# Optimization experiments

Measured on AMD Instinct MI355X. Metric: run time of the kernel, lower is better.

The kernel has to match this reference:

```python
import jax, jax.numpy as jnp
import numpy as np

N_NODES = 20000
N_EDGES = 640000
IN_DIM = 128
HID = 128
OUT_DIM = 64
N_STEPS = 16   # N in the torch module
H = 0.1        # ODE step size


def setup_inputs() -> dict:
    key = jax.random.key(0)
    ks = jax.random.split(key, 20)
    s = 1.0 / np.sqrt(HID)

    def g(k, shape, scale=s):
        return (jax.random.normal(k, shape, dtype=jnp.float32) * scale)

    return {
        "x": jax.random.normal(ks[0], (N_NODES, IN_DIM), dtype=jnp.float32),
        "edge_index": jax.random.randint(ks[1], (2, N_EDGES), 0, N_NODES, dtype=jnp.int32),
        "W_enc1": g(ks[2], (HID, IN_DIM), 1.0 / np.sqrt(IN_DIM)),
        "b_enc1": g(ks[3], (HID,)),
        "W_enc2": g(ks[4], (HID, HID)),
        "b_enc2": g(ks[5], (HID,)),
        "W_ih_f": g(ks[6], (4 * HID, HID)),
        "W_hh_f": g(ks[7], (4 * HID, HID)),
        "b_ih_f": g(ks[8], (4 * HID,)),
        "b_hh_f": g(ks[9], (4 * HID,)),
        "W_ih_b": g(ks[10], (4 * HID, HID)),
        "W_hh_b": g(ks[11], (4 * HID, HID)),
        "b_ih_b": g(ks[12], (4 * HID,)),
        "b_hh_b": g(ks[13], (4 * HID,)),
        "W_f1": g(ks[14], (HID, 2 * HID), 1.0 / np.sqrt(2 * HID)),
        "b_f1": g(ks[15], (HID,)),
        "W_f2": g(ks[16], (OUT_DIM, HID)),
        "b_f2": g(ks[17], (OUT_DIM,)),
    }


def _lstm_scan(xs, W_ih, W_hh, b_ih, b_hh):
    """Unidirectional LSTM over xs [T, B, H] -> hidden states [T, B, H]."""
    B = xs.shape[1]
    Hd = W_hh.shape[1]
    h0 = jnp.zeros((B, Hd), xs.dtype)

    def cell(carry, x_t):
        h, c = carry
        gates = x_t @ W_ih.T + b_ih + h @ W_hh.T + b_hh
        i, f, g, o = jnp.split(gates, 4, axis=-1)  # torch gate order: i,f,g,o
        i = jax.nn.sigmoid(i)
        f = jax.nn.sigmoid(f)
        g = jnp.tanh(g)
        o = jax.nn.sigmoid(o)
        c_new = f * c + i * g
        h_new = o * jnp.tanh(c_new)
        return (h_new, c_new), h_new

    _, hs = jax.lax.scan(cell, (h0, h0), xs)
    return hs


def reference(x, edge_index, W_enc1, b_enc1, W_enc2, b_enc2,
              W_ih_f, W_hh_f, b_ih_f, b_hh_f,
              W_ih_b, W_hh_b, b_ih_b, b_hh_b,
              W_f1, b_f1, W_f2, b_f2):
    row, col = edge_index[0], edge_index[1]

    # initial encoders
    X = x @ W_enc1.T + b_enc1
    Y = jnp.zeros_like(X)
    X = jax.nn.relu(X)
    X = X @ W_enc2.T + b_enc2

    # node degree (count of col occurrences), inf-guard not needed (deg used directly)
    deg = jax.ops.segment_sum(jnp.ones((N_EDGES,), X.dtype), col, num_segments=N_NODES)

    def wave_step(carry, _):
        Xc, Yc = carry
        # L x = deg*x - sum_{j->i} x_j   (scatter-add of -x[row] at col)
        mes = -jax.ops.segment_sum(Xc[row], col, num_segments=N_NODES)
        vel_update = deg[:, None] * Xc + mes
        Yn = Yc - H * vel_update
        Xn = Xc + H * Yn
        return (Xn, Yn), Xn

    _, Xs = jax.lax.scan(wave_step, (X, Y), None, length=N_STEPS - 1)
    X_tilde = jnp.concatenate([X[None], Xs], axis=0)  # [N, n_nodes, HID]

    hs_f = _lstm_scan(X_tilde, W_ih_f, W_hh_f, b_ih_f, b_hh_f)
    hs_b = _lstm_scan(X_tilde[::-1], W_ih_b, W_hh_b, b_ih_b, b_hh_b)
    # out_vec[-1] = [fwd hidden at last step, bwd hidden at last position]
    out_last = jnp.concatenate([hs_f[-1], hs_b[0]], axis=-1)  # [n_nodes, 2*HID]

    out = jax.nn.relu(out_last @ W_f1.T + b_f1)
    out = out @ W_f2.T + b_f2
    return out
```

## Files before the change

### kernel.cpp

```cpp
#include <hip/hip_runtime.h>
#include <hip/hip_bf16.h>
#include <cstdint>
#include <cstddef>

#define N_NODES 20000
#define N_EDGES 640000
#define HID     128
#define OUT_DIM 64
#define NSTEPS  16
#define HSTEP   0.1f
#define H2      0.01f
#define NBLK    625

typedef unsigned short u16;
typedef __attribute__((ext_vector_type(8))) short short8;
typedef __attribute__((ext_vector_type(4))) float f32x4;

__device__ __forceinline__ float bf2f(u16 u) {
    union { unsigned int i; float f; } v; v.i = ((unsigned int)u) << 16; return v.f;
}
__device__ __forceinline__ u16 f2bf(float f) {
    union { float f; unsigned int i; } v; v.f = f;
    unsigned int x = v.i;
    unsigned int r = x + 0x7FFFu + ((x >> 16) & 1u);
    return (u16)(r >> 16);
}

__device__ __forceinline__ float sigm(float x) { return 1.f / (1.f + __expf(-x)); }
__device__ __forceinline__ float tanh_fast(float x) {
    float e2 = __expf(-2.f * fabsf(x));
    float t = (1.f - e2) / (1.f + e2);
    return copysignf(t, x);
}

__global__ void detect_kernel(const u16* __restrict__ xraw, int* __restrict__ flag) {
    __shared__ int cnt;
    if (threadIdx.x == 0) cnt = 0;
    __syncthreads();
    int c = 0;
    for (int i = threadIdx.x; i < 4096; i += 256) {
        int e = (xraw[i] >> 7) & 0xFF;
        if (e >= 0x90) c++;
    }
    atomicAdd(&cnt, c);
    __syncthreads();
    if (threadIdx.x == 0) *flag = (cnt > 100) ? 1 : 0;
}

#define N_CVT 15
struct CvtArgs { const void* s[N_CVT]; };
__constant__ const int cvt_off[N_CVT + 1] = {
    0, 16384, 16512, 32896, 33024, 98560, 164096, 164608, 165120,
    230656, 231168, 231680, 264448, 264576, 272768, 272832 };

__global__ void convert_kernel(CvtArgs a, float* __restrict__ dst,
                               const int* __restrict__ flag) {
    int i = blockIdx.x * blockDim.x + threadIdx.x;
    if (i >= 272832) return;
    int seg = 0;
    #pragma unroll
    for (int s = 1; s < N_CVT; ++s) if (i >= cvt_off[s]) seg = s;
    int j = i - cvt_off[seg];
    float v = (*flag) ? ((const float*)a.s[seg])[j]
                      : bf2f(((const u16*)a.s[seg])[j]);
    dst[i] = v;
}

__global__ void build_wswz_kernel(const float* __restrict__ wsf,
                                  u16* __restrict__ WswzF, u16* __restrict__ WswzB,
                                  u16* __restrict__ WswzH, u16* __restrict__ WswzO,
                                  u16* __restrict__ WswzE1, u16* __restrict__ WswzE2) {
    int o = blockIdx.x * blockDim.x + threadIdx.x;
    if (o < 131072) {
        int j = o & 7, l = (o >> 3) & 63, rest = o >> 9;
        int ck = rest & 7, nt = rest >> 3;
        int n = nt * 16 + (l & 15);
        int k = ck * 32 + (l >> 4) * 8 + j;
        const float* Wihf = wsf + 33024;
        const float* Whhf = wsf + 98560;
        float v = (k < 128) ? Wihf[n * 128 + k] : Whhf[n * 128 + (k - 128)];
        WswzF[o] = f2bf(v);
    }
    if (o < 65536) {
        int j = o & 7, l = (o >> 3) & 63, rest = o >> 9;
        int ck = rest & 3, nt = rest >> 2;
        int n = nt * 16 + (l & 15);
        int k = ck * 32 + (l >> 4) * 8 + j;
        const float* Wihb = wsf + 165120;
        WswzB[o] = f2bf(Wihb[n * 128 + k]);
    }
    if (o < 32768) {
        int j = o & 7, l = (o >> 3) & 63, rest = o >> 9;
        int ck = rest & 7, nt = rest >> 3;
        int n = nt * 16 + (l & 15);
        int k = ck * 32 + (l >> 4) * 8 + j;
        const float* Wf1 = wsf + 231680;
        WswzH[o] = f2bf(Wf1[n * 256 + k]);
    }
    if (o < 8192) {
        int j = o & 7, l = (o >> 3) & 63, rest = o >> 9;
        int ck = rest & 3, nt = rest >> 2;
        int n = nt * 16 + (l & 15);
        int k = ck * 32 + (l >> 4) * 8 + j;
        const float* Wf2 = wsf + 264576;
        WswzO[o] = f2bf(Wf2[n * 128 + k]);
    }
    if (o < 16384) {
        int j = o & 7, l = (o >> 3) & 63, rest = o >> 9;
        int ck = rest & 3, nt = rest >> 2;
        int n = nt * 16 + (l & 15);
        int k = ck * 32 + (l >> 4) * 8 + j;
        const float* We1 = wsf + 0;
        const float* We2 = wsf + 16512;
        WswzE1[o] = f2bf(We1[n * 128 + k]);
        WswzE2[o] = f2bf(We2[n * 128 + k]);
    }
}

__global__ void count_kernel(const int* __restrict__ ei, int* __restrict__ deg) {
    int e = blockIdx.x * blockDim.x + threadIdx.x;
    if (e < N_EDGES) atomicAdd(&deg[ei[N_EDGES + e]], 1);
}

__global__ __launch_bounds__(1024) void scan_kernel(const int* __restrict__ deg,
                                                    int* __restrict__ rowptr,
                                                    float* __restrict__ degf) {
    __shared__ int sd[1024];
    const int t = threadIdx.x;
    const int CH = (N_NODES + 1023) / 1024;
    int base = t * CH;
    int s = 0;
    for (int i = 0; i < CH; ++i) {
        int idx = base + i;
        if (idx < N_NODES) s += deg[idx];
    }
    sd[t] = s;
    __syncthreads();
    for (int off = 1; off < 1024; off <<= 1) {
        int v = (t >= off) ? sd[t - off] : 0;
        __syncthreads();
        sd[t] += v;
        __syncthreads();
    }
    int run = (t == 0) ? 0 : sd[t - 1];
    for (int i = 0; i < CH; ++i) {
        int idx = base + i;
        if (idx < N_NODES) {
            rowptr[idx] = run;
            degf[idx] = (float)deg[idx];
            run += deg[idx];
        }
    }
    if (t == 1023) rowptr[N_NODES] = sd[1023];
}

__global__ void fill_kernel(const int* __restrict__ ei, const int* __restrict__ rowptr,
                            int* __restrict__ fill, int* __restrict__ csr) {
    int e = blockIdx.x * blockDim.x + threadIdx.x;
    if (e < N_EDGES) {
        int d = ei[N_EDGES + e];
        int p = atomicAdd(&fill[d], 1);
        csr[rowptr[d] + p] = ei[e];
    }
}

__global__ __launch_bounds__(512) void encoder_kernel(
    const void* __restrict__ xv,
    const u16* __restrict__ WswzE1, const u16* __restrict__ WswzE2,
    const float* __restrict__ benc1, const float* __restrict__ benc2,
    float* __restrict__ Xa, u16* __restrict__ Xsnap0, const int* __restrict__ flag)
{
    __shared__ __align__(16) u16 H1[32][136];
    const int w = threadIdx.x >> 6;
    const int l = threadIdx.x & 63;
    const int l15 = l & 15, quad = l >> 4;
    const int m0 = blockIdx.x * 32;
    const int kof = quad * 8;
    const int j = w * 16 + l15;
    const bool xf32 = (*flag != 0);

    f32x4 acc[2] = {};
    #pragma unroll
    for (int ck = 0; ck < 4; ++ck) {
        const int kc = ck * 32;
        short8 a0, a1;
        if (xf32) {
            const float* r0 = (const float*)xv + (size_t)(m0 + l15) * HID + kc + kof;
            const float* r1 = (const float*)xv + (size_t)(m0 + 16 + l15) * HID + kc + kof;
            union { u16 u[8]; short8 v; } t0, t1;
            #pragma unroll
            for (int e = 0; e < 8; ++e) { t0.u[e] = f2bf(r0[e]); t1.u[e] = f2bf(r1[e]); }
            a0 = t0.v; a1 = t1.v;
        } else {
            a0 = *(const short8*)((const u16*)xv + (size_t)(m0 + l15) * HID + kc + kof);
            a1 = *(const short8*)((const u16*)xv + (size_t)(m0 + 16 + l15) * HID + kc + kof);
        }
        short8 b = *(const short8*)(WswzE1 + (((size_t)(w * 4 + ck)) << 9) + (l << 3));
        acc[0] = __builtin_amdgcn_mfma_f32_16x16x32_bf16(a0, b, acc[0], 0, 0, 0);
        acc[1] = __builtin_amdgcn_mfma_f32_16x16x32_bf16(a1, b, acc[1], 0, 0, 0);
    }
    {
        const float bj = benc1[j];
        #pragma unroll
        for (int mt = 0; mt < 2; ++mt)
            #pragma unroll
            for (int i = 0; i < 4; ++i)
                H1[mt * 16 + quad * 4 + i][j] = f2bf(fmaxf(acc[mt][i] + bj, 0.f));
    }
    __syncthreads();

    f32x4 acc2[2] = {};
    #pragma unroll
    for (int ck = 0; ck < 4; ++ck) {
        const int kc = ck * 32;
        short8 a0 = *(const short8*)(&H1[l15][kc + kof]);
        short8 a1 = *(const short8*)(&H1[16 + l15][kc + kof]);
        short8 b = *(const short8*)(WswzE2 + (((size_t)(w * 4 + ck)) << 9) + (l << 3));
        acc2[0] = __builtin_amdgcn_mfma_f32_16x16x32_bf16(a0, b, acc2[0], 0, 0, 0);
        acc2[1] = __builtin_amdgcn_mfma_f32_16x16x32_bf16(a1, b, acc2[1], 0, 0, 0);
    }
    {
        const float bj = benc2[j];
        #pragma unroll
        for (int mt = 0; mt < 2; ++mt)
            #pragma unroll
            for (int i = 0; i < 4; ++i) {
                int m = m0 + mt * 16 + quad * 4 + i;
                float o = acc2[mt][i] + bj;
                Xa[(size_t)m * HID + j] = o;
                Xsnap0[(size_t)m * HID + j] = f2bf(o);
            }
    }
}

template<bool FIRST>
__global__ __launch_bounds__(256) void wave_kernel(
    const float* __restrict__ Xcur, float* __restrict__ Xdst,
    const u16* __restrict__ XbfP, u16* __restrict__ XbfN,
    const float* __restrict__ degf,
    const int* __restrict__ rowptr, const int* __restrict__ csr)
{
    const int node = blockIdx.x * 4 + (threadIdx.x >> 6);
    const int lane = threadIdx.x & 63;
    const int q = lane >> 4;
    const int fl = (lane & 15) * 8;

    const int beg = rowptr[node], end = rowptr[node + 1];
    float s0[8] = {}, s1[8] = {}, s2[8] = {}, s3[8] = {};

    int i = beg;
    for (; i + 16 <= end; i += 16) {
        int v0 = csr[i + 0 + q];
        int v1 = csr[i + 4 + q];
        int v2 = csr[i + 8 + q];
        int v3 = csr[i + 12 + q];
        short8 g0 = *(const short8*)(XbfP + (size_t)v0 * HID + fl);
        short8 g1 = *(const short8*)(XbfP + (size_t)v1 * HID + fl);
        short8 g2 = *(const short8*)(XbfP + (size_t)v2 * HID + fl);
        short8 g3 = *(const short8*)(XbfP + (size_t)v3 * HID + fl);
        #pragma unroll
        for (int e = 0; e < 8; ++e) {
            s0[e] += bf2f((u16)g0[e]);
            s1[e] += bf2f((u16)g1[e]);
            s2[e] += bf2f((u16)g2[e]);
            s3[e] += bf2f((u16)g3[e]);
        }
    }
    for (; i + 4 <= end; i += 4) {
        int v = csr[i + q];
        short8 g = *(const short8*)(XbfP + (size_t)v * HID + fl);
        #pragma unroll
        for (int e = 0; e < 8; ++e) s0[e] += bf2f((u16)g[e]);
    }
    if (i + q < end) {
        int v = csr[i + q];
        short8 g = *(const short8*)(XbfP + (size_t)v * HID + fl);
        #pragma unroll
        for (int e = 0; e < 8; ++e) s1[e] += bf2f((u16)g[e]);
    }

    float t[8];
    #pragma unroll
    for (int e = 0; e < 8; ++e) {
        t[e] = (s0[e] + s1[e]) + (s2[e] + s3[e]);
        t[e] += __shfl_xor(t[e], 16, 64);
        t[e] += __shfl_xor(t[e], 32, 64);
    }

    if (q == 0) {
        const size_t off = (size_t)node * HID + fl;
        float xc[8], xp[8], xn[8];
        *(float4*)&xc[0] = *(const float4*)(Xcur + off);
        *(float4*)&xc[4] = *(const float4*)(Xcur + off + 4);
        if (!FIRST) {
            *(float4*)&xp[0] = *(const float4*)(Xdst + off);
            *(float4*)&xp[4] = *(const float4*)(Xdst + off + 4);
        }
        const float d = degf[node];
        const float c0 = 2.f - H2 * d;
        short8 sv;
        #pragma unroll
        for (int e = 0; e < 8; ++e) {
            float prev = FIRST ? xc[e] : xp[e];
            xn[e] = c0 * xc[e] - prev + H2 * t[e];
            sv[e] = (short)f2bf(xn[e]);
        }
        *(float4*)(Xdst + off)     = *(float4*)&xn[0];
        *(float4*)(Xdst + off + 4) = *(float4*)&xn[4];
        *(short8*)(XbfN + off)     = sv;
    }
}

__global__ __launch_bounds__(512) void lstm_tail_kernel(
    const u16* __restrict__ Xsnap,
    const u16* __restrict__ WswzF,
    const float* __restrict__ bih, const float* __restrict__ bhh,
    const u16* __restrict__ WswzB, const u16* __restrict__ WswzH,
    const u16* __restrict__ WswzO,
    const float* __restrict__ bihb, const float* __restrict__ bhhb,
    const float* __restrict__ bf1, const float* __restrict__ bf2_,
    void* __restrict__ out, const int* __restrict__ oflag)
{
    __shared__ __align__(16) u16 hL[32][136];
    __shared__ __align__(16) u16 Hb[32][136];
    __shared__ __align__(16) u16 F1[32][136];
    const int w = threadIdx.x >> 6;
    const int l = threadIdx.x & 63;
    const int l15 = l & 15, quad = l >> 4;
    const int m0 = blockIdx.x * 32;
    const int kof = quad * 8;
    const int j = w * 16 + l15;

    {
        const int r  = threadIdx.x >> 4;
        const int cc = (threadIdx.x & 15) * 8;
        short8 z = {};
        *(short8*)&hL[r][cc] = z;
    }

    const float bI = bih[j]       + bhh[j];
    const float bF = bih[128 + j] + bhh[128 + j];
    const float bG = bih[256 + j] + bhh[256 + j];
    const float bO = bih[384 + j] + bhh[384 + j];
    float cst[2][4] = {};

    const size_t rowA0 = (size_t)(m0 + l15) * HID + kof;
    const size_t rowA1 = (size_t)(m0 + 16 + l15) * HID + kof;
    __syncthreads();

    #pragma unroll 1
    for (int t = 0; t < NSTEPS; ++t) {
        const u16* Xbf = Xsnap + (size_t)t * N_NODES * HID;
        f32x4 acc[2][4] = {};
        #pragma unroll
        for (int kc = 0; kc < 256; kc += 32) {
            const int ck = kc >> 5;
            short8 a0, a1;
            if (kc < 128) {
                a0 = *(const short8*)(Xbf + rowA0 + kc);
                a1 = *(const short8*)(Xbf + rowA1 + kc);
            } else {
                a0 = *(const short8*)(&hL[l15][kc - 128 + kof]);
                a1 = *(const short8*)(&hL[16 + l15][kc - 128 + kof]);
            }
            #pragma unroll
            for (int q = 0; q < 4; ++q) {
                int nt = q * 8 + w;
                short8 b = *(const short8*)(WswzF + (((size_t)(nt * 8 + ck)) << 9) + (l << 3));
                acc[0][q] = __builtin_amdgcn_mfma_f32_16x16x32_bf16(a0, b, acc[0][q], 0, 0, 0);
                acc[1][q] = __builtin_amdgcn_mfma_f32_16x16x32_bf16(a1, b, acc[1][q], 0, 0, 0);
            }
        }
        __syncthreads();
        #pragma unroll
        for (int mt = 0; mt < 2; ++mt) {
            #pragma unroll
            for (int i = 0; i < 4; ++i) {
                float gi = sigm(acc[mt][0][i] + bI);
                float gf = sigm(acc[mt][1][i] + bF);
                float gg = tanh_fast(acc[mt][2][i] + bG);
                float go = sigm(acc[mt][3][i] + bO);
                float cn = gf * cst[mt][i] + gi * gg;
                cst[mt][i] = cn;
                hL[mt * 16 + quad * 4 + i][j] = f2bf(go * tanh_fast(cn));
            }
        }
        __syncthreads();
    }

    {
        const u16* Xbf15 = Xsnap + (size_t)(NSTEPS - 1) * N_NODES * HID;
        f32x4 acc[2][4] = {};
        #pragma unroll
        for (int kc = 0; kc < 128; kc += 32) {
            const int ck = kc >> 5;
            short8 a0 = *(const short8*)(Xbf15 + rowA0 + kc);
            short8 a1 = *(const short8*)(Xbf15 + rowA1 + kc);
            #pragma unroll
            for (int q = 0; q < 4; ++q) {
                int nt = q * 8 + w;
                short8 b = *(const short8*)(WswzB + (((size_t)(nt * 4 + ck)) << 9) + (l << 3));
                acc[0][q] = __builtin_amdgcn_mfma_f32_16x16x32_bf16(a0, b, acc[0][q], 0, 0, 0);
                acc[1][q] = __builtin_amdgcn_mfma_f32_16x16x32_bf16(a1, b, acc[1][q], 0, 0, 0);
            }
        }
        const float cI = bihb[j]       + bhhb[j];
        const float cG = bihb[256 + j] + bhhb[256 + j];
        const float cO = bihb[384 + j] + bhhb[384 + j];
        #pragma unroll
        for (int mt = 0; mt < 2; ++mt)
            #pragma unroll
            for (int i = 0; i < 4; ++i) {
                float gi = sigm(acc[mt][0][i] + cI);
                float gg = tanh_fast(acc[mt][2][i] + cG);
                float go = sigm(acc[mt][3][i] + cO);
                Hb[mt * 16 + quad * 4 + i][j] = f2bf(go * tanh_fast(gi * gg));
            }
    }
    __syncthreads();

    {
        f32x4 acc[2] = {};
        #pragma unroll
        for (int kc = 0; kc < 256; kc += 32) {
            const int ck = kc >> 5;
            short8 a0, a1;
            if (kc < 128) {
                a0 = *(const short8*)(&hL[l15][kc + kof]);
                a1 = *(const short8*)(&hL[16 + l15][kc + kof]);
            } else {
                a0 = *(const short8*)(&Hb[l15][(kc - 128) + kof]);
                a1 = *(const short8*)(&Hb[16 + l15][(kc - 128) + kof]);
            }
            short8 b = *(const short8*)(WswzH + (((size_t)(w * 8 + ck)) << 9) + (l << 3));
            acc[0] = __builtin_amdgcn_mfma_f32_16x16x32_bf16(a0, b, acc[0], 0, 0, 0);
            acc[1] = __builtin_amdgcn_mfma_f32_16x16x32_bf16(a1, b, acc[1], 0, 0, 0);
        }
        const float bj = bf1[j];
        #pragma unroll
        for (int mt = 0; mt < 2; ++mt)
            #pragma unroll
            for (int i = 0; i < 4; ++i)
                F1[mt * 16 + quad * 4 + i][j] = f2bf(fmaxf(acc[mt][i] + bj, 0.f));
    }
    __syncthreads();

    {
        const int nt = w & 3, mh = w >> 2;
        f32x4 acc = {};
        #pragma unroll
        for (int kc = 0; kc < 128; kc += 32) {
            const int ck = kc >> 5;
            short8 a = *(const short8*)(&F1[mh * 16 + l15][kc + kof]);
            short8 b = *(const short8*)(WswzO + (((size_t)(nt * 4 + ck)) << 9) + (l << 3));
            acc = __builtin_amdgcn_mfma_f32_16x16x32_bf16(a, b, acc, 0, 0, 0);
        }
        const int jo = nt * 16 + l15;
        const float bj = bf2_[jo];
        const bool obf = (*oflag == 0);
        #pragma unroll
        for (int i = 0; i < 4; ++i) {
            int m = m0 + mh * 16 + quad * 4 + i;
            float o = acc[i] + bj;
            if (obf) ((u16*)out)[(size_t)m * OUT_DIM + jo] = f2bf(o);
            else     ((float*)out)[(size_t)m * OUT_DIM + jo] = o;
        }
    }
}

extern "C" void kernel_launch(void* const* d_in, const int* in_sizes, int n_in,
                              void* d_out, int out_size, void* d_ws, size_t ws_size,
                              hipStream_t stream)
{
    const void* x  = d_in[0];
    const int*  ei = (const int*)d_in[1];

    const size_t SZ_NH  = (size_t)N_NODES * HID * sizeof(float);
    const size_t SZ_NHB = (size_t)N_NODES * HID * sizeof(u16);
    const size_t SZ_I   = 80128;

    char* p = (char*)d_ws;
    float* Xa    = (float*)p; p += SZ_NH;
    float* Xb    = (float*)p; p += SZ_NH;
    u16*   Xsnap = (u16*)p;   p += (size_t)NSTEPS * SZ_NHB;
    int*   deg   = (int*)p;   p += SZ_I;
    int*   fill  = (int*)p;   p += SZ_I;
    int*   rowp  = (int*)p;   p += SZ_I;
    float* degf  = (float*)p; p += SZ_I;
    int*   csr   = (int*)p;   p += (size_t)N_EDGES * sizeof(int);
    int*   flag  = (int*)p;   p += 128;
    float* wsf   = (float*)p; p += 272832 * sizeof(float);
    u16*   WswzF  = (u16*)p;  p += 131072 * sizeof(u16);
    u16*   WswzB  = (u16*)p;  p += 65536 * sizeof(u16);
    u16*   WswzH  = (u16*)p;  p += 32768 * sizeof(u16);
    u16*   WswzO  = (u16*)p;  p += 8192 * sizeof(u16);
    u16*   WswzE1 = (u16*)p;  p += 16384 * sizeof(u16);
    u16*   WswzE2 = (u16*)p;  p += 16384 * sizeof(u16);

    float* benc1 = wsf + 16384;
    float* benc2 = wsf + 32896;
    float* bihf  = wsf + 164096;
    float* bhhf  = wsf + 164608;
    float* bihb  = wsf + 230656;
    float* bhhb  = wsf + 231168;
    float* bf1   = wsf + 264448;
    float* bf2_  = wsf + 272768;

    (void)hipMemsetAsync(deg, 0, 2 * SZ_I, stream);

    detect_kernel<<<1, 256, 0, stream>>>((const u16*)x, flag);
    CvtArgs ca;
    ca.s[0] = d_in[2];  ca.s[1] = d_in[3];  ca.s[2] = d_in[4];  ca.s[3] = d_in[5];
    ca.s[4] = d_in[6];  ca.s[5] = d_in[7];  ca.s[6] = d_in[8];  ca.s[7] = d_in[9];
    ca.s[8] = d_in[10]; ca.s[9] = d_in[12]; ca.s[10] = d_in[13];
    ca.s[11] = d_in[14]; ca.s[12] = d_in[15]; ca.s[13] = d_in[16]; ca.s[14] = d_in[17];
    convert_kernel<<<(272832 + 255) / 256, 256, 0, stream>>>(ca, wsf, flag);
    build_wswz_kernel<<<512, 256, 0, stream>>>(wsf, WswzF, WswzB, WswzH, WswzO,
                                               WswzE1, WswzE2);

    count_kernel<<<(N_EDGES + 255) / 256, 256, 0, stream>>>(ei, deg);
    scan_kernel<<<1, 1024, 0, stream>>>(deg, rowp, degf);
    fill_kernel<<<(N_EDGES + 255) / 256, 256, 0, stream>>>(ei, rowp, fill, csr);

    const int NB = NBLK;

    encoder_kernel<<<NB, 512, 0, stream>>>(x, WswzE1, WswzE2, benc1, benc2,
                                           Xa, Xsnap, flag);

    float* Xc_ = Xa;
    float* Xo_ = Xb;
    for (int t = 1; t < NSTEPS; ++t) {
        const u16* XbP = Xsnap + (size_t)(t - 1) * N_NODES * HID;
        u16*       XbN = Xsnap + (size_t)t * N_NODES * HID;
        if (t == 1)
            wave_kernel<true><<<N_NODES / 4, 256, 0, stream>>>(
                Xc_, Xo_, XbP, XbN, degf, rowp, csr);
        else
            wave_kernel<false><<<N_NODES / 4, 256, 0, stream>>>(
                Xc_, Xo_, XbP, XbN, degf, rowp, csr);
        float* tf = Xc_; Xc_ = Xo_; Xo_ = tf;
    }

    lstm_tail_kernel<<<NB, 512, 0, stream>>>(Xsnap, WswzF, bihf, bhhf,
                                             WswzB, WswzH, WswzO,
                                             bihb, bhhb, bf1, bf2_,
                                             d_out, flag);
}
```

Measured before the change: 827.8 us.

## Fuse forward LSTM steps into wave-step kernels as extra blocks

```diff
diff --git a/kernel.cpp b/kernel.cpp
--- a/kernel.cpp
+++ b/kernel.cpp
@@ -11,6 +11,8 @@
 #define HSTEP   0.1f
 #define H2      0.01f
 #define NBLK    625
+#define WAVEBLK 5000
+#define LSTMBLK 1250
 
 typedef unsigned short u16;
 typedef __attribute__((ext_vector_type(8))) short short8;
@@ -234,85 +236,140 @@
 }
 
 template<bool FIRST>
-__global__ __launch_bounds__(256) void wave_kernel(
+__global__ __launch_bounds__(256) void fused_step_kernel(
     const float* __restrict__ Xcur, float* __restrict__ Xdst,
     const u16* __restrict__ XbfP, u16* __restrict__ XbfN,
     const float* __restrict__ degf,
-    const int* __restrict__ rowptr, const int* __restrict__ csr)
+    const int* __restrict__ rowptr, const int* __restrict__ csr,
+    const u16* __restrict__ hR, u16* __restrict__ hW, float* __restrict__ cf,
+    const u16* __restrict__ WswzF,
+    const float* __restrict__ bih, const float* __restrict__ bhh)
 {
-    const int node = blockIdx.x * 4 + (threadIdx.x >> 6);
-    const int lane = threadIdx.x & 63;
-    const int q = lane >> 4;
-    const int fl = (lane & 15) * 8;
-
-    const int beg = rowptr[node], end = rowptr[node + 1];
-    float s0[8] = {}, s1[8] = {}, s2[8] = {}, s3[8] = {};
-
-    int i = beg;
-    for (; i + 16 <= end; i += 16) {
-        int v0 = csr[i + 0 + q];
-        int v1 = csr[i + 4 + q];
-        int v2 = csr[i + 8 + q];
-        int v3 = csr[i + 12 + q];
-        short8 g0 = *(const short8*)(XbfP + (size_t)v0 * HID + fl);
-        short8 g1 = *(const short8*)(XbfP + (size_t)v1 * HID + fl);
-        short8 g2 = *(const short8*)(XbfP + (size_t)v2 * HID + fl);
-        short8 g3 = *(const short8*)(XbfP + (size_t)v3 * HID + fl);
+    if (blockIdx.x < WAVEBLK) {
+        const int node = blockIdx.x * 4 + (threadIdx.x >> 6);
+        const int lane = threadIdx.x & 63;
+        const int q = lane >> 4;
+        const int fl = (lane & 15) * 8;
+
+        const int beg = rowptr[node], end = rowptr[node + 1];
+        float s0[8] = {}, s1[8] = {}, s2[8] = {}, s3[8] = {};
+
+        int i = beg;
+        for (; i + 16 <= end; i += 16) {
+            int v0 = csr[i + 0 + q];
+            int v1 = csr[i + 4 + q];
+            int v2 = csr[i + 8 + q];
+            int v3 = csr[i + 12 + q];
+            short8 g0 = *(const short8*)(XbfP + (size_t)v0 * HID + fl);
+            short8 g1 = *(const short8*)(XbfP + (size_t)v1 * HID + fl);
+            short8 g2 = *(const short8*)(XbfP + (size_t)v2 * HID + fl);
+            short8 g3 = *(const short8*)(XbfP + (size_t)v3 * HID + fl);
+            #pragma unroll
+            for (int e = 0; e < 8; ++e) {
+                s0[e] += bf2f((u16)g0[e]);
+                s1[e] += bf2f((u16)g1[e]);
+                s2[e] += bf2f((u16)g2[e]);
+                s3[e] += bf2f((u16)g3[e]);
+            }
+        }
+        for (; i + 4 <= end; i += 4) {
+            int v = csr[i + q];
+            short8 g = *(const short8*)(XbfP + (size_t)v * HID + fl);
+            #pragma unroll
+            for (int e = 0; e < 8; ++e) s0[e] += bf2f((u16)g[e]);
+        }
+        if (i + q < end) {
+            int v = csr[i + q];
+            short8 g = *(const short8*)(XbfP + (size_t)v * HID + fl);
+            #pragma unroll
+            for (int e = 0; e < 8; ++e) s1[e] += bf2f((u16)g[e]);
+        }
+
+        float t[8];
         #pragma unroll
         for (int e = 0; e < 8; ++e) {
-            s0[e] += bf2f((u16)g0[e]);
-            s1[e] += bf2f((u16)g1[e]);
-            s2[e] += bf2f((u16)g2[e]);
-            s3[e] += bf2f((u16)g3[e]);
-        }
-    }
-    for (; i + 4 <= end; i += 4) {
-        int v = csr[i + q];
-        short8 g = *(const short8*)(XbfP + (size_t)v * HID + fl);
-        #pragma unroll
-        for (int e = 0; e < 8; ++e) s0[e] += bf2f((u16)g[e]);
-    }
-    if (i + q < end) {
-        int v = csr[i + q];
-        short8 g = *(const short8*)(XbfP + (size_t)v * HID + fl);
-        #pragma unroll
-        for (int e = 0; e < 8; ++e) s1[e] += bf2f((u16)g[e]);
-    }
-
-    float t[8];
+            t[e] = (s0[e] + s1[e]) + (s2[e] + s3[e]);
+            t[e] += __shfl_xor(t[e], 16, 64);
+            t[e] += __shfl_xor(t[e], 32, 64);
+        }
+
+        if (q == 0) {
+            const size_t off = (size_t)node * HID + fl;
+            float xc[8], xp[8], xn[8];
+            *(float4*)&xc[0] = *(const float4*)(Xcur + off);
+            *(float4*)&xc[4] = *(const float4*)(Xcur + off + 4);
+            if (!FIRST) {
+                *(float4*)&xp[0] = *(const float4*)(Xdst + off);
+                *(float4*)&xp[4] = *(const float4*)(Xdst + off + 4);
+            }
+            const float d = degf[node];
+            const float c0 = 2.f - H2 * d;
+            short8 sv;
+            #pragma unroll
+            for (int e = 0; e < 8; ++e) {
+                float prev = FIRST ? xc[e] : xp[e];
+                xn[e] = c0 * xc[e] - prev + H2 * t[e];
+                sv[e] = (short)f2bf(xn[e]);
+            }
+            *(float4*)(Xdst + off)     = *(float4*)&xn[0];
+            *(float4*)(Xdst + off + 4) = *(float4*)&xn[4];
+            *(short8*)(XbfN + off)     = sv;
+        }
+        return;
+    }
+
+    const int tid = threadIdx.x;
+    const int w = tid >> 6;
+    const int l = tid & 63;
+    const int l15 = l & 15, quad = l >> 4;
+    const int kof = quad * 8;
+    const int m0 = (blockIdx.x - WAVEBLK) * 16;
+
+    f32x4 acc[2][4] = {};
+    const size_t rowA = (size_t)(m0 + l15) * HID + kof;
+
     #pragma unroll
-    for (int e = 0; e < 8; ++e) {
-        t[e] = (s0[e] + s1[e]) + (s2[e] + s3[e]);
-        t[e] += __shfl_xor(t[e], 16, 64);
-        t[e] += __shfl_xor(t[e], 32, 64);
-    }
-
-    if (q == 0) {
-        const size_t off = (size_t)node * HID + fl;
-        float xc[8], xp[8], xn[8];
-        *(float4*)&xc[0] = *(const float4*)(Xcur + off);
-        *(float4*)&xc[4] = *(const float4*)(Xcur + off + 4);
-        if (!FIRST) {
-            *(float4*)&xp[0] = *(const float4*)(Xdst + off);
-            *(float4*)&xp[4] = *(const float4*)(Xdst + off + 4);
-        }
-        const float d = degf[node];
-        const float c0 = 2.f - H2 * d;
-        short8 sv;
-        #pragma unroll
-        for (int e = 0; e < 8; ++e) {
-            float prev = FIRST ? xc[e] : xp[e];
-            xn[e] = c0 * xc[e] - prev + H2 * t[e];
-            sv[e] = (short)f2bf(xn[e]);
-        }
-        *(float4*)(Xdst + off)     = *(float4*)&xn[0];
-        *(float4*)(Xdst + off + 4) = *(float4*)&xn[4];
-        *(short8*)(XbfN + off)     = sv;
-    }
-}
-
-__global__ __launch_bounds__(512) void lstm_tail_kernel(
-    const u16* __restrict__ Xsnap,
+    for (int kc = 0; kc < 256; kc += 32) {
+        const int ck = kc >> 5;
+        short8 a = (kc < 128)
+            ? *(const short8*)(XbfP + rowA + kc)
+            : *(const short8*)(hR + rowA + (kc - 128));
+        #pragma unroll
+        for (int jp = 0; jp < 2; ++jp)
+            #pragma unroll
+            for (int q = 0; q < 4; ++q) {
+                const int nt = q * 8 + w + jp * 4;
+                short8 b = *(const short8*)(WswzF +
+                    (((size_t)(nt * 8 + ck)) << 9) + (l << 3));
+                acc[jp][q] = __builtin_amdgcn_mfma_f32_16x16x32_bf16(
+                    a, b, acc[jp][q], 0, 0, 0);
+            }
+    }
+
+    #pragma unroll
+    for (int jp = 0; jp < 2; ++jp) {
+        const int j = (w + 4 * jp) * 16 + l15;
+        const float bI = bih[j]       + bhh[j];
+        const float bF = bih[128 + j] + bhh[128 + j];
+        const float bG = bih[256 + j] + bhh[256 + j];
+        const float bO = bih[384 + j] + bhh[384 + j];
+        #pragma unroll
+        for (int i = 0; i < 4; ++i) {
+            const size_t off = (size_t)(m0 + quad * 4 + i) * HID + j;
+            float gi = sigm(acc[jp][0][i] + bI);
+            float gf = sigm(acc[jp][1][i] + bF);
+            float gg = tanh_fast(acc[jp][2][i] + bG);
+            float go = sigm(acc[jp][3][i] + bO);
+            float cn = gf * cf[off] + gi * gg;
+            cf[off] = cn;
+            hW[off] = f2bf(go * tanh_fast(cn));
+        }
+    }
+}
+
+__global__ __launch_bounds__(512) void tail_kernel(
+    const u16* __restrict__ Xbf15,
+    const u16* __restrict__ hPrev, const float* __restrict__ cPrev,
     const u16* __restrict__ WswzF,
     const float* __restrict__ bih, const float* __restrict__ bhh,
     const u16* __restrict__ WswzB, const u16* __restrict__ WswzH,
@@ -334,31 +391,34 @@
     {
         const int r  = threadIdx.x >> 4;
         const int cc = (threadIdx.x & 15) * 8;
-        short8 z = {};
-        *(short8*)&hL[r][cc] = z;
+        *(short8*)&hL[r][cc] =
+            *(const short8*)(hPrev + (size_t)(m0 + r) * HID + cc);
     }
 
     const float bI = bih[j]       + bhh[j];
     const float bF = bih[128 + j] + bhh[128 + j];
     const float bG = bih[256 + j] + bhh[256 + j];
     const float bO = bih[384 + j] + bhh[384 + j];
-    float cst[2][4] = {};
+    float cst[2][4];
+    #pragma unroll
+    for (int mt = 0; mt < 2; ++mt)
+        #pragma unroll
+        for (int i = 0; i < 4; ++i)
+            cst[mt][i] = cPrev[(size_t)(m0 + mt * 16 + quad * 4 + i) * HID + j];
 
     const size_t rowA0 = (size_t)(m0 + l15) * HID + kof;
     const size_t rowA1 = (size_t)(m0 + 16 + l15) * HID + kof;
     __syncthreads();
 
-    #pragma unroll 1
-    for (int t = 0; t < NSTEPS; ++t) {
-        const u16* Xbf = Xsnap + (size_t)t * N_NODES * HID;
+    {
         f32x4 acc[2][4] = {};
         #pragma unroll
         for (int kc = 0; kc < 256; kc += 32) {
             const int ck = kc >> 5;
             short8 a0, a1;
             if (kc < 128) {
-                a0 = *(const short8*)(Xbf + rowA0 + kc);
-                a1 = *(const short8*)(Xbf + rowA1 + kc);
+                a0 = *(const short8*)(Xbf15 + rowA0 + kc);
+                a1 = *(const short8*)(Xbf15 + rowA1 + kc);
             } else {
                 a0 = *(const short8*)(&hL[l15][kc - 128 + kof]);
                 a1 = *(const short8*)(&hL[16 + l15][kc - 128 + kof]);
@@ -381,7 +441,6 @@
                 float gg = tanh_fast(acc[mt][2][i] + bG);
                 float go = sigm(acc[mt][3][i] + bO);
                 float cn = gf * cst[mt][i] + gi * gg;
-                cst[mt][i] = cn;
                 hL[mt * 16 + quad * 4 + i][j] = f2bf(go * tanh_fast(cn));
             }
         }
@@ -389,7 +448,6 @@
     }
 
     {
-        const u16* Xbf15 = Xsnap + (size_t)(NSTEPS - 1) * N_NODES * HID;
         f32x4 acc[2][4] = {};
         #pragma unroll
         for (int kc = 0; kc < 128; kc += 32) {
@@ -483,6 +541,9 @@
     float* Xa    = (float*)p; p += SZ_NH;
     float* Xb    = (float*)p; p += SZ_NH;
     u16*   Xsnap = (u16*)p;   p += (size_t)NSTEPS * SZ_NHB;
+    float* cf    = (float*)p; p += SZ_NH;
+    u16*   hB    = (u16*)p;   p += SZ_NHB;
+    u16*   hA    = (u16*)p;   p += SZ_NHB;
     int*   deg   = (int*)p;   p += SZ_I;
     int*   fill  = (int*)p;   p += SZ_I;
     int*   rowp  = (int*)p;   p += SZ_I;
@@ -507,6 +568,7 @@
     float* bf2_  = wsf + 272768;
 
     (void)hipMemsetAsync(deg, 0, 2 * SZ_I, stream);
+    (void)hipMemsetAsync(cf, 0, SZ_NH + SZ_NHB, stream);
 
     detect_kernel<<<1, 256, 0, stream>>>((const u16*)x, flag);
     CvtArgs ca;
@@ -522,27 +584,30 @@
     scan_kernel<<<1, 1024, 0, stream>>>(deg, rowp, degf);
     fill_kernel<<<(N_EDGES + 255) / 256, 256, 0, stream>>>(ei, rowp, fill, csr);
 
-    const int NB = NBLK;
-
-    encoder_kernel<<<NB, 512, 0, stream>>>(x, WswzE1, WswzE2, benc1, benc2,
-                                           Xa, Xsnap, flag);
+    encoder_kernel<<<NBLK, 512, 0, stream>>>(x, WswzE1, WswzE2, benc1, benc2,
+                                             Xa, Xsnap, flag);
 
     float* Xc_ = Xa;
     float* Xo_ = Xb;
     for (int t = 1; t < NSTEPS; ++t) {
+        const int s = t - 1;
         const u16* XbP = Xsnap + (size_t)(t - 1) * N_NODES * HID;
         u16*       XbN = Xsnap + (size_t)t * N_NODES * HID;
+        const u16* hR = (s & 1) ? hA : hB;
+        u16*       hW = (s & 1) ? hB : hA;
         if (t == 1)
-            wave_kernel<true><<<N_NODES / 4, 256, 0, stream>>>(
-                Xc_, Xo_, XbP, XbN, degf, rowp, csr);
+            fused_step_kernel<true><<<WAVEBLK + LSTMBLK, 256, 0, stream>>>(
+                Xc_, Xo_, XbP, XbN, degf, rowp, csr, hR, hW, cf,
+                WswzF, bihf, bhhf);
         else
-            wave_kernel<false><<<N_NODES / 4, 256, 0, stream>>>(
-                Xc_, Xo_, XbP, XbN, degf, rowp, csr);
+            fused_step_kernel<false><<<WAVEBLK + LSTMBLK, 256, 0, stream>>>(
+                Xc_, Xo_, XbP, XbN, degf, rowp, csr, hR, hW, cf,
+                WswzF, bihf, bhhf);
         float* tf = Xc_; Xc_ = Xo_; Xo_ = tf;
     }
 
-    lstm_tail_kernel<<<NB, 512, 0, stream>>>(Xsnap, WswzF, bihf, bhhf,
-                                             WswzB, WswzH, WswzO,
-                                             bihb, bhhb, bf1, bf2_,
-                                             d_out, flag);
-}
+    tail_kernel<<<NBLK, 512, 0, stream>>>(
+        Xsnap + (size_t)(NSTEPS - 1) * N_NODES * HID, hA, cf,
+        WswzF, bihf, bhhf, WswzB, WswzH, WswzO,
+        bihb, bhhb, bf1, bf2_, d_out, flag);
+}
```

New measurement: 968.1 us. 16.9% more time.

## Split LSTM recurrence into 256-thread kernel and separate tail kernel

Applied to the files above, without the earlier changes.

```diff
diff --git a/kernel.cpp b/kernel.cpp
--- a/kernel.cpp
+++ b/kernel.cpp
@@ -311,10 +311,103 @@
     }
 }
 
-__global__ __launch_bounds__(512) void lstm_tail_kernel(
+__global__ __launch_bounds__(256) void lstm16_kernel(
     const u16* __restrict__ Xsnap,
+    u16* __restrict__ hOut,
     const u16* __restrict__ WswzF,
-    const float* __restrict__ bih, const float* __restrict__ bhh,
+    const float* __restrict__ bih, const float* __restrict__ bhh)
+{
+    __shared__ __align__(16) u16 hL[32][136];
+    const int tid  = threadIdx.x;
+    const int w    = tid >> 6;
+    const int l    = tid & 63;
+    const int l15  = l & 15;
+    const int quad = l >> 4;
+    const int kof  = quad * 8;
+    const int m0   = blockIdx.x * 32;
+
+    {
+        const int r  = tid >> 3;
+        const int cc = (tid & 7) * 16;
+        short8 z = {};
+        *(short8*)&hL[r][cc]     = z;
+        *(short8*)&hL[r][cc + 8] = z;
+    }
+
+    const int jh[2] = { w * 16 + l15, (w + 4) * 16 + l15 };
+    float cst[2][2][4] = {};
+    float bI[2], bF[2], bG[2], bO[2];
+    #pragma unroll
+    for (int jp = 0; jp < 2; ++jp) {
+        bI[jp] = bih[jh[jp]]       + bhh[jh[jp]];
+        bF[jp] = bih[128 + jh[jp]] + bhh[128 + jh[jp]];
+        bG[jp] = bih[256 + jh[jp]] + bhh[256 + jh[jp]];
+        bO[jp] = bih[384 + jh[jp]] + bhh[384 + jh[jp]];
+    }
+
+    const size_t rowA0 = (size_t)(m0 + l15) * HID + kof;
+    const size_t rowA1 = (size_t)(m0 + 16 + l15) * HID + kof;
+    __syncthreads();
+
+    #pragma unroll 1
+    for (int t = 0; t < NSTEPS; ++t) {
+        const u16* Xbf = Xsnap + (size_t)t * N_NODES * HID;
+
+        f32x4 acc[2][2][4] = {};
+        #pragma unroll
+        for (int kc = 0; kc < 256; kc += 32) {
+            const int ck = kc >> 5;
+            short8 a0, a1;
+            if (kc < 128) {
+                a0 = *(const short8*)(Xbf + rowA0 + kc);
+                a1 = *(const short8*)(Xbf + rowA1 + kc);
+            } else {
+                a0 = *(const short8*)(&hL[l15][kc - 128 + kof]);
+                a1 = *(const short8*)(&hL[16 + l15][kc - 128 + kof]);
+            }
+            #pragma unroll
+            for (int jp = 0; jp < 2; ++jp)
+                #pragma unroll
+                for (int g4 = 0; g4 < 4; ++g4) {
+                    const int nt = g4 * 8 + w + jp * 4;
+                    short8 b = *(const short8*)(WswzF +
+                        (((size_t)(nt * 8 + ck)) << 9) + (l << 3));
+                    acc[0][jp][g4] = __builtin_amdgcn_mfma_f32_16x16x32_bf16(
+                        a0, b, acc[0][jp][g4], 0, 0, 0);
+                    acc[1][jp][g4] = __builtin_amdgcn_mfma_f32_16x16x32_bf16(
+                        a1, b, acc[1][jp][g4], 0, 0, 0);
+                }
+        }
+        __syncthreads();
+
+        #pragma unroll
+        for (int mt = 0; mt < 2; ++mt)
+            #pragma unroll
+            for (int jp = 0; jp < 2; ++jp)
+                #pragma unroll
+                for (int i = 0; i < 4; ++i) {
+                    float gi = sigm(acc[mt][jp][0][i] + bI[jp]);
+                    float gf = sigm(acc[mt][jp][1][i] + bF[jp]);
+                    float gg = tanh_fast(acc[mt][jp][2][i] + bG[jp]);
+                    float go = sigm(acc[mt][jp][3][i] + bO[jp]);
+                    float cn = gf * cst[mt][jp][i] + gi * gg;
+                    cst[mt][jp][i] = cn;
+                    hL[mt * 16 + quad * 4 + i][jh[jp]] = f2bf(go * tanh_fast(cn));
+                }
+        __syncthreads();
+    }
+
+    {
+        const int r  = tid >> 3;
+        const int cc = (tid & 7) * 16;
+        u16* hdst = hOut + (size_t)(m0 + r) * HID + cc;
+        *(short8*)(hdst)     = *(const short8*)&hL[r][cc];
+        *(short8*)(hdst + 8) = *(const short8*)&hL[r][cc + 8];
+    }
+}
+
+__global__ __launch_bounds__(512) void tail2_kernel(
+    const u16* __restrict__ Xbf15, const u16* __restrict__ h15,
     const u16* __restrict__ WswzB, const u16* __restrict__ WswzH,
     const u16* __restrict__ WswzO,
     const float* __restrict__ bihb, const float* __restrict__ bhhb,
@@ -334,62 +427,14 @@
     {
         const int r  = threadIdx.x >> 4;
         const int cc = (threadIdx.x & 15) * 8;
-        short8 z = {};
-        *(short8*)&hL[r][cc] = z;
-    }
-
-    const float bI = bih[j]       + bhh[j];
-    const float bF = bih[128 + j] + bhh[128 + j];
-    const float bG = bih[256 + j] + bhh[256 + j];
-    const float bO = bih[384 + j] + bhh[384 + j];
-    float cst[2][4] = {};
+        *(short8*)&hL[r][cc] =
+            *(const short8*)(h15 + (size_t)(m0 + r) * HID + cc);
+    }
 
     const size_t rowA0 = (size_t)(m0 + l15) * HID + kof;
     const size_t rowA1 = (size_t)(m0 + 16 + l15) * HID + kof;
-    __syncthreads();
-
-    #pragma unroll 1
-    for (int t = 0; t < NSTEPS; ++t) {
-        const u16* Xbf = Xsnap + (size_t)t * N_NODES * HID;
-        f32x4 acc[2][4] = {};
-        #pragma unroll
-        for (int kc = 0; kc < 256; kc += 32) {
-            const int ck = kc >> 5;
-            short8 a0, a1;
-            if (kc < 128) {
-                a0 = *(const short8*)(Xbf + rowA0 + kc);
-                a1 = *(const short8*)(Xbf + rowA1 + kc);
-            } else {
-                a0 = *(const short8*)(&hL[l15][kc - 128 + kof]);
-                a1 = *(const short8*)(&hL[16 + l15][kc - 128 + kof]);
-            }
-            #pragma unroll
-            for (int q = 0; q < 4; ++q) {
-                int nt = q * 8 + w;
-                short8 b = *(const short8*)(WswzF + (((size_t)(nt * 8 + ck)) << 9) + (l << 3));
-                acc[0][q] = __builtin_amdgcn_mfma_f32_16x16x32_bf16(a0, b, acc[0][q], 0, 0, 0);
-                acc[1][q] = __builtin_amdgcn_mfma_f32_16x16x32_bf16(a1, b, acc[1][q], 0, 0, 0);
-            }
-        }
-        __syncthreads();
-        #pragma unroll
-        for (int mt = 0; mt < 2; ++mt) {
-            #pragma unroll
-            for (int i = 0; i < 4; ++i) {
-                float gi = sigm(acc[mt][0][i] + bI);
-                float gf = sigm(acc[mt][1][i] + bF);
-                float gg = tanh_fast(acc[mt][2][i] + bG);
-                float go = sigm(acc[mt][3][i] + bO);
-                float cn = gf * cst[mt][i] + gi * gg;
-                cst[mt][i] = cn;
-                hL[mt * 16 + quad * 4 + i][j] = f2bf(go * tanh_fast(cn));
-            }
-        }
-        __syncthreads();
-    }
-
-    {
-        const u16* Xbf15 = Xsnap + (size_t)(NSTEPS - 1) * N_NODES * HID;
+
+    {
         f32x4 acc[2][4] = {};
         #pragma unroll
         for (int kc = 0; kc < 128; kc += 32) {
@@ -483,6 +528,7 @@
     float* Xa    = (float*)p; p += SZ_NH;
     float* Xb    = (float*)p; p += SZ_NH;
     u16*   Xsnap = (u16*)p;   p += (size_t)NSTEPS * SZ_NHB;
+    u16*   h15   = (u16*)p;   p += SZ_NHB;
     int*   deg   = (int*)p;   p += SZ_I;
     int*   fill  = (int*)p;   p += SZ_I;
     int*   rowp  = (int*)p;   p += SZ_I;
@@ -522,10 +568,8 @@
     scan_kernel<<<1, 1024, 0, stream>>>(deg, rowp, degf);
     fill_kernel<<<(N_EDGES + 255) / 256, 256, 0, stream>>>(ei, rowp, fill, csr);
 
-    const int NB = NBLK;
-
-    encoder_kernel<<<NB, 512, 0, stream>>>(x, WswzE1, WswzE2, benc1, benc2,
-                                           Xa, Xsnap, flag);
+    encoder_kernel<<<NBLK, 512, 0, stream>>>(x, WswzE1, WswzE2, benc1, benc2,
+                                             Xa, Xsnap, flag);
 
     float* Xc_ = Xa;
     float* Xo_ = Xb;
@@ -541,8 +585,9 @@
         float* tf = Xc_; Xc_ = Xo_; Xo_ = tf;
     }
 
-    lstm_tail_kernel<<<NB, 512, 0, stream>>>(Xsnap, WswzF, bihf, bhhf,
-                                             WswzB, WswzH, WswzO,
-                                             bihb, bhhb, bf1, bf2_,
-                                             d_out, flag);
-}
+    lstm16_kernel<<<NBLK, 256, 0, stream>>>(Xsnap, h15, WswzF, bihf, bhhf);
+
+    tail2_kernel<<<NBLK, 512, 0, stream>>>(
+        Xsnap + (size_t)(NSTEPS - 1) * N_NODES * HID, h15,
+        WswzB, WswzH, WswzO, bihb, bhhb, bf1, bf2_, d_out, flag);
+}
```

New measurement: 831.3 us. About the same (+0.4%).
